# Kernel optimization log

Hardware: AMD Instinct MI355X
Metric: run time of the kernel (lower is better)

## Reference

```python
import jax, jax.numpy as jnp
import numpy as np

NUM_HEADS = 8
N_MOD = 3


def _sinusoidal_pe(seq_len, d_model):
    # standard sinusoidal table [seq_len, d_model]
    pos = np.arange(seq_len, dtype=np.float32)[:, None]
    div = np.exp(np.arange(0, d_model, 2, dtype=np.float32) * (-np.log(10000.0) / d_model))
    pe = np.zeros((seq_len, d_model), dtype=np.float32)
    pe[:, 0::2] = np.sin(pos * div)
    pe[:, 1::2] = np.cos(pos * div)
    return jnp.asarray(pe)


def _attn_mask(dim_x, dim_z, n_mod):
    # additive mask [dim_x, dim_x + n_mod*dim_z]: 0 where allowed, -inf elsewhere
    blocks = [np.eye(dim_x, dtype=np.float32)]
    for _ in range(n_mod):  # all modalities present (mod_list == full_mod)
        p2 = np.zeros((dim_x, dim_z), dtype=np.float32)
        p2[dim_x - dim_z:, :] = np.eye(dim_z, dtype=np.float32)
        blocks.append(p2)
    m = np.concatenate(blocks, axis=1)
    return jnp.asarray(np.where(m < 1, -np.inf, 0.0).astype(np.float32))


def setup_inputs() -> dict:
    key = jax.random.key(0)
    ks = jax.random.split(key, 8)
    bs, en, dx, dz = 32, 256, 512, 256
    state = jax.random.normal(ks[0], (bs, en, dx), jnp.float32)
    obs0 = jax.random.normal(ks[1], (bs, en, dz), jnp.float32)
    obs1 = jax.random.normal(ks[2], (bs, en, dz), jnp.float32)
    obs2 = jax.random.normal(ks[3], (bs, en, dz), jnp.float32)
    Q = jax.random.uniform(ks[4], (dx, en), jnp.float32)  # torch.rand init
    Wq = jax.random.normal(ks[5], (en, en), jnp.float32) / np.sqrt(en)
    Wk = jax.random.normal(ks[6], (en, en), jnp.float32) / np.sqrt(en)
    bq = jnp.zeros((en,), jnp.float32)
    bk = jnp.zeros((en,), jnp.float32)
    return {"state": state, "obs0": obs0, "obs1": obs1, "obs2": obs2,
            "Q": Q, "Wq": Wq, "bq": bq, "Wk": Wk, "bk": bk}


def reference(state, obs0, obs1, obs2, Q, Wq, bq, Wk, bk):
    bs, en, dx = state.shape
    dz = obs0.shape[2]
    obs_list = (obs0, obs1, obs2)
    mask = _attn_mask(dx, dz, N_MOD)            # [dx, L]
    pe = _sinusoidal_pe(bs, en)                 # positions run over batch axis (faithful quirk)

    # mean-center over the ensemble axis
    A = state - jnp.mean(state, axis=1, keepdims=True)          # [bs, en, dx]
    Ys = [o - jnp.mean(o, axis=1, keepdims=True) for o in obs_list]

    # build query / key-value sequences in [tokens, bs, en] layout, add PE, then batch-major
    q = Q[:, None, :] + pe[None, :, :]                          # [dx, bs, en]
    xy = jnp.concatenate([jnp.transpose(A, (2, 0, 1))]
                         + [jnp.transpose(Y, (2, 0, 1)) for Y in Ys], axis=0)
    xy = xy + pe[None, :, :]                                    # [L, bs, en]
    qb = jnp.transpose(q, (1, 0, 2))                            # [bs, dx, en]
    kb = jnp.transpose(xy, (1, 0, 2))                           # [bs, L, en]

    # multi-head masked attention (output path is discarded by the original module,
    # only the attention map is used, so no V/O projection is needed)
    dh = en // NUM_HEADS
    qh = (qb @ Wq + bq).reshape(bs, dx, NUM_HEADS, dh).transpose(0, 2, 1, 3)   # [bs,h,dx,dh]
    kh = (kb @ Wk + bk).reshape(bs, -1, NUM_HEADS, dh).transpose(0, 2, 1, 3)   # [bs,h,L,dh]
    scores = jnp.einsum('bhqd,bhkd->bhqk', qh, kh) / np.sqrt(dh).astype(np.float32)
    scores = scores + mask[None, None, :, :]
    atten = jnp.mean(jax.nn.softmax(scores, axis=-1), axis=1)   # [bs, dx, L]

    # attn-weighted matmul over concatenated raw state+obs
    merge = jnp.concatenate([state, obs0, obs1, obs2], axis=2)  # [bs, en, L]
    new_state = jnp.einsum('bql,bel->beq', atten, merge)        # [bs, en, dx]
    return new_state, atten
```

## Files before the change

kernel.cpp:

```cpp
#include <hip/hip_runtime.h>
#include <math.h>


__global__ __launch_bounds__(256)
void k_uv_copy(const float* __restrict__ Q, const float* __restrict__ Wq,
               const float* __restrict__ bq, const float* __restrict__ state,
               float* __restrict__ uT, float* __restrict__ vT,
               float* __restrict__ out0) {
  const int blk = blockIdx.x;
  const int t = threadIdx.x;
  if (blk < 288) {
    __shared__ float row[256];
    float rv;
    if (blk < 256) {
      rv = Q[(256 + blk) * 256 + t];
    } else {
      const int b = blk - 256;
      const float dv = expf(-9.210340371976184f * (float)((t >> 1) << 1) * (1.0f / 256.0f));
      const float ang = (float)b * dv;
      rv = (t & 1) ? cosf(ang) : sinf(ang);
    }
    row[t] = rv;
    __syncthreads();
    float acc = (blk < 256) ? 0.0f : bq[t];
    for (int e = 0; e < 256; ++e) acc += row[e] * Wq[e * 256 + t];
    if (blk < 256) uT[t * 256 + blk] = acc;
    else           vT[t * 32 + (blk - 256)] = acc;
  } else {
    const int id = blk - 288;
    const int b = id >> 5, eg = id & 31;
    const int r = t >> 5;
    const int c = t & 31;
    const int e = eg * 8 + r;
    const size_t base = ((size_t)(b * 256 + e)) * 512;
    *(float4*)(out0 + base + c * 4)        = *(const float4*)(state + base + c * 4);
    *(float4*)(out0 + base + (c + 32) * 4) = *(const float4*)(state + base + (c + 32) * 4);
  }
}

__global__ __launch_bounds__(256)
void k_w(const float* __restrict__ Wk, const float* __restrict__ uT,
         const float* __restrict__ vT, float* __restrict__ wu2,
         float* __restrict__ wv) {
  const int blk = blockIdx.x;
  const int t = threadIdx.x;
  const int e = blk & 255;
  const int part = blk >> 8;
  __shared__ float wrow[256];
  wrow[t] = Wk[e * 256 + t];
  __syncthreads();
  if (part == 0) {
#pragma unroll
    for (int h = 0; h < 8; ++h) {
      float acc = 0.0f;
#pragma unroll
      for (int d = 0; d < 32; ++d)
        acc += uT[(h * 32 + d) * 256 + t] * wrow[h * 32 + d];
      wu2[(size_t)(h * 256 + e) * 272 + t] = acc;
    }
  } else if (t < 32) {
#pragma unroll
    for (int h = 0; h < 8; ++h) {
      float acc = 0.0f;
#pragma unroll
      for (int d = 0; d < 32; ++d)
        acc += vT[(h * 32 + d) * 32 + t] * wrow[h * 32 + d];
      wv[(t * 8 + h) * 256 + e] = acc;
    }
  }
}

__global__ __launch_bounds__(512)
void k_all(const float* __restrict__ state, const float* __restrict__ o0,
           const float* __restrict__ o1, const float* __restrict__ o2,
           const float* __restrict__ wu2, const float* __restrict__ wv,
           float* __restrict__ out0, float* __restrict__ out1) {
  const int t = threadIdx.x;
  const int jt = blockIdx.x;
  const int b  = blockIdx.y;

  __shared__ float s_data[4][128][17];
  __shared__ float s_wvb[2048];
  __shared__ float s_part[8][16][25];
  __shared__ float s_tot[44][16];
  __shared__ float s_a[16][4];

  for (int i = t; i < 2048; i += 512) s_wvb[i] = wv[b * 2048 + i];

  const int jl = t & 15;
  const int es = (t >> 4) & 15;
  const int hp = t >> 8;
  const int j = jt * 16 + jl;

  float acc[24];
#pragma unroll
  for (int k = 0; k < 24; ++k) acc[k] = 0.f;

  const float* pwu = wu2 + (size_t)hp * 4 * 256 * 272 + j;
  const float* pwvb = s_wvb + hp * 4 * 256;

#pragma unroll
  for (int chunk = 0; chunk < 2; ++chunk) {
    __syncthreads();
#pragma unroll
    for (int rep = 0; rep < 4; ++rep) {
      const int c = t + rep * 512;
      const int m = c >> 9;
      const int r = c & 511;
      const int e = r >> 2;
      const int jq = r & 3;
      const int ge = chunk * 128 + e;
      const int j0 = jt * 16 + jq * 4;
      const float* src;
      if (m == 0)      src = state + ((size_t)(b * 256 + ge)) * 512 + 256 + j0;
      else if (m == 1) src = o0 + ((size_t)(b * 256 + ge)) * 256 + j0;
      else if (m == 2) src = o1 + ((size_t)(b * 256 + ge)) * 256 + j0;
      else             src = o2 + ((size_t)(b * 256 + ge)) * 256 + j0;
      const float4 v4 = *(const float4*)src;
      const int jb = jq * 4;
      s_data[m][e][jb]   = v4.x; s_data[m][e][jb+1] = v4.y;
      s_data[m][e][jb+2] = v4.z; s_data[m][e][jb+3] = v4.w;
    }
    __syncthreads();

#pragma unroll
    for (int it = 0; it < 8; ++it) {
      const int el = it * 16 + es;
      const int e = chunk * 128 + el;
      const float s  = s_data[0][el][jl];
      const float x0 = s_data[1][el][jl];
      const float x1 = s_data[2][el][jl];
      const float x2 = s_data[3][el][jl];
      acc[20] += s; acc[21] += x0; acc[22] += x1; acc[23] += x2;
#pragma unroll
      for (int hh = 0; hh < 4; ++hh) {
        const float w = pwu[(size_t)(hh * 256 + e) * 272] + pwvb[hh * 256 + e];
        acc[hh * 5 + 0] += s * w;  acc[hh * 5 + 1] += x0 * w;
        acc[hh * 5 + 2] += x1 * w; acc[hh * 5 + 3] += x2 * w;
        acc[hh * 5 + 4] += w;
      }
    }
  }

#pragma unroll
  for (int k = 0; k < 24; ++k) {
    acc[k] += __shfl_xor(acc[k], 16);
    acc[k] += __shfl_xor(acc[k], 32);
  }
  if ((t & 48) == 0) {
    const int w = t >> 6;
    float* p = &s_part[w][jl][0];
#pragma unroll
    for (int k = 0; k < 24; ++k) p[k] = acc[k];
  }
  __syncthreads();

  if (t < 16) {
#pragma unroll
    for (int k = 0; k < 20; ++k)
      s_tot[k][t] = s_part[0][t][k] + s_part[1][t][k] + s_part[2][t][k] + s_part[3][t][k];
#pragma unroll
    for (int c = 0; c < 4; ++c)
      s_tot[40 + c][t] = s_part[0][t][20 + c] + s_part[1][t][20 + c] +
                         s_part[2][t][20 + c] + s_part[3][t][20 + c];
  } else if (t >= 256 && t < 272) {
    const int l = t & 15;
#pragma unroll
    for (int k = 0; k < 20; ++k)
      s_tot[20 + k][l] = s_part[4][l][k] + s_part[5][l][k] + s_part[6][l][k] + s_part[7][l][k];
  }
  __syncthreads();

  if (t < 16) {
    float tot[44];
#pragma unroll
    for (int k = 0; k < 44; ++k) tot[k] = s_tot[k][t];
    const float m0 = tot[40] * (1.f / 256.f), m1 = tot[41] * (1.f / 256.f);
    const float m2 = tot[42] * (1.f / 256.f), m3 = tot[43] * (1.f / 256.f);
    const float inv = 0.17677669529663687f;
    float am0 = 0.f, am1 = 0.f, am2 = 0.f, am3 = 0.f;
#pragma unroll
    for (int h = 0; h < 8; ++h) {
      const float dO = tot[h * 5 + 4];
      const float s0 = (tot[h * 5 + 0] - m0 * dO) * inv;
      const float s1 = (tot[h * 5 + 1] - m1 * dO) * inv;
      const float s2 = (tot[h * 5 + 2] - m2 * dO) * inv;
      const float s3 = (tot[h * 5 + 3] - m3 * dO) * inv;
      const float mx = fmaxf(fmaxf(s0, s1), fmaxf(s2, s3));
      const float e0 = expf(s0 - mx), e1 = expf(s1 - mx);
      const float e2 = expf(s2 - mx), e3 = expf(s3 - mx);
      const float r = 1.f / (e0 + e1 + e2 + e3);
      am0 += e0 * r; am1 += e1 * r; am2 += e2 * r; am3 += e3 * r;
    }
    s_a[t][0] = am0 * 0.125f; s_a[t][1] = am1 * 0.125f;
    s_a[t][2] = am2 * 0.125f; s_a[t][3] = am3 * 0.125f;
  }
  __syncthreads();

  {
    const int jl2 = t & 15;
    const int er = t >> 4;
    const float a0 = s_a[jl2][0], a1 = s_a[jl2][1];
    const float a2 = s_a[jl2][2], a3 = s_a[jl2][3];
    const int jj = jt * 16 + jl2;
#pragma unroll
    for (int k = 0; k < 4; ++k) {
      const int e = er + 32 * k;
      const size_t idxS = ((size_t)(b * 256 + e)) * 512 + 256 + jj;
      const size_t idxO = ((size_t)(b * 256 + e)) * 256 + jj;
      out0[idxS] = a0 * state[idxS] + a1 * o0[idxO] + a2 * o1[idxO] + a3 * o2[idxO];
    }
#pragma unroll
    for (int k = 4; k < 8; ++k) {
      const int e = er + 32 * k;
      const int el = e - 128;
      const size_t idxS = ((size_t)(b * 256 + e)) * 512 + 256 + jj;
      out0[idxS] = a0 * s_data[0][el][jl2] + a1 * s_data[1][el][jl2] +
                   a2 * s_data[2][el][jl2] + a3 * s_data[3][el][jl2];
    }
  }

  {
    const int r = t >> 5;
    const int c = t & 31;
    const int j3 = jt * 16 + r;
    const int q = 256 + j3;
    const int comp = j3 & 3;
    const int tc0 = (256 + j3) >> 2, tc1 = (512 + j3) >> 2;
    const int tc2 = (768 + j3) >> 2, tc3 = (1024 + j3) >> 2;
    const float av0 = s_a[r][0], av1 = s_a[r][1];
    const float av2 = s_a[r][2], av3 = s_a[r][3];
    float4* orow = (float4*)(out1 + ((size_t)(b * 512 + q)) * 1280);
#pragma unroll
    for (int k = 0; k < 10; ++k) {
      const int c4 = c + 32 * k;
      float4 o = make_float4(0.f, 0.f, 0.f, 0.f);
      float val = 0.f; bool hit = false;
      if (c4 == tc0)      { val = av0; hit = true; }
      else if (c4 == tc1) { val = av1; hit = true; }
      else if (c4 == tc2) { val = av2; hit = true; }
      else if (c4 == tc3) { val = av3; hit = true; }
      if (hit) {
        if (comp == 0) o.x = val; else if (comp == 1) o.y = val;
        else if (comp == 2) o.z = val; else o.w = val;
      }
      orow[c4] = o;
    }
  }

  {
    const int r = t >> 5;
    const int c = t & 31;
    const int q = jt * 16 + r;
    const int tq = q >> 2;
    const int comp = q & 3;
    float4* orow = (float4*)(out1 + ((size_t)(b * 512 + q)) * 1280);
#pragma unroll
    for (int k = 0; k < 10; ++k) {
      const int c4 = c + 32 * k;
      float4 o = make_float4(0.f, 0.f, 0.f, 0.f);
      if (c4 == tq) {
        if (comp == 0) o.x = 1.f; else if (comp == 1) o.y = 1.f;
        else if (comp == 2) o.z = 1.f; else o.w = 1.f;
      }
      orow[c4] = o;
    }
  }
}

extern "C" void kernel_launch(void* const* d_in, const int* in_sizes, int n_in,
                              void* d_out, int out_size, void* d_ws, size_t ws_size,
                              hipStream_t stream) {
  const float* state = (const float*)d_in[0];
  const float* obs0  = (const float*)d_in[1];
  const float* obs1  = (const float*)d_in[2];
  const float* obs2  = (const float*)d_in[3];
  const float* Q     = (const float*)d_in[4];
  const float* Wq    = (const float*)d_in[5];
  const float* bq    = (const float*)d_in[6];
  const float* Wk    = (const float*)d_in[7];

  float* out0 = (float*)d_out;
  float* out1 = out0 + (size_t)32 * 256 * 512;

  float* ws  = (float*)d_ws;
  float* uT  = ws;
  float* vT  = uT + 65536;
  float* wu2 = vT + 8192;
  float* wv  = wu2 + 557056;

  k_uv_copy<<<1312, 256, 0, stream>>>(Q, Wq, bq, state, uT, vT, out0);
  k_w<<<512, 256, 0, stream>>>(Wk, uT, vT, wu2, wv);
  k_all<<<dim3(16, 32), 512, 0, stream>>>(state, obs0, obs1, obs2, wu2, wv, out0, out1);
}
```

Baseline: 60.66 us.

## Pre-transpose state/obs data to bf16 so the main kernel loads a compact layout

Adds a preprocessing stage in the first kernel that converts the state tail and the three observation tensors to bf16 and transposes them so the ensemble axis is contiguous. The main kernel then loads all 256 ensemble rows for its tile in one pass from this compact buffer, drops the two-chunk reload loop, and computes the weighted output from bf16 values held in shared memory. The intent is to halve the bytes the main kernel reads and to make those loads coalesced. In exchange the first kernel does an extra full read and write pass, and both the scores and the final new_state output are computed from bf16-rounded inputs, which loses precision.

New measurement: 56.70 us. 6.5% less time.

```diff
diff --git a/kernel.cpp b/kernel.cpp
--- a/kernel.cpp
+++ b/kernel.cpp
@@ -1,12 +1,23 @@
 #include <hip/hip_runtime.h>
 #include <math.h>
 
+
+__device__ inline unsigned short f2bf(float f) {
+  unsigned int x = __float_as_uint(f);
+  x += 0x7fffu + ((x >> 16) & 1u);
+  return (unsigned short)(x >> 16);
+}
+__device__ inline float bf2f(unsigned short s) {
+  return __uint_as_float(((unsigned int)s) << 16);
+}
 
 __global__ __launch_bounds__(256)
 void k_uv_copy(const float* __restrict__ Q, const float* __restrict__ Wq,
                const float* __restrict__ bq, const float* __restrict__ state,
+               const float* __restrict__ o0, const float* __restrict__ o1,
+               const float* __restrict__ o2,
                float* __restrict__ uT, float* __restrict__ vT,
-               float* __restrict__ out0) {
+               unsigned short* __restrict__ dT, float* __restrict__ out0) {
   const int blk = blockIdx.x;
   const int t = threadIdx.x;
   if (blk < 288) {
@@ -26,7 +37,7 @@
     for (int e = 0; e < 256; ++e) acc += row[e] * Wq[e * 256 + t];
     if (blk < 256) uT[t * 256 + blk] = acc;
     else           vT[t * 32 + (blk - 256)] = acc;
-  } else {
+  } else if (blk < 1312) {
     const int id = blk - 288;
     const int b = id >> 5, eg = id & 31;
     const int r = t >> 5;
@@ -35,6 +46,41 @@
     const size_t base = ((size_t)(b * 256 + e)) * 512;
     *(float4*)(out0 + base + c * 4)        = *(const float4*)(state + base + c * 4);
     *(float4*)(out0 + base + (c + 32) * 4) = *(const float4*)(state + base + (c + 32) * 4);
+  } else {
+    const int id = blk - 1312;
+    const int b   = id >> 6;
+    const int m   = (id >> 4) & 3;
+    const int jt4 = (id >> 2) & 3;
+    const int et4 = id & 3;
+    __shared__ unsigned short tile[64][72];
+    const float* srcb;
+    int stride, colbase;
+    if (m == 0)      { srcb = state + ((size_t)b * 256) * 512; stride = 512; colbase = 256 + jt4 * 64; }
+    else if (m == 1) { srcb = o0 + ((size_t)b * 256) * 256; stride = 256; colbase = jt4 * 64; }
+    else if (m == 2) { srcb = o1 + ((size_t)b * 256) * 256; stride = 256; colbase = jt4 * 64; }
+    else             { srcb = o2 + ((size_t)b * 256) * 256; stride = 256; colbase = jt4 * 64; }
+#pragma unroll
+    for (int rep = 0; rep < 4; ++rep) {
+      const int c = t + rep * 256;
+      const int f4 = c & 15;
+      const int row = c >> 4;
+      const float4 v = *(const float4*)(srcb + (size_t)(et4 * 64 + row) * stride + colbase + f4 * 4);
+      tile[row][f4 * 4 + 0] = f2bf(v.x); tile[row][f4 * 4 + 1] = f2bf(v.y);
+      tile[row][f4 * 4 + 2] = f2bf(v.z); tile[row][f4 * 4 + 3] = f2bf(v.w);
+    }
+    __syncthreads();
+#pragma unroll
+    for (int rep = 0; rep < 2; ++rep) {
+      const int c = t + rep * 256;
+      const int oct = c & 7;
+      const int jrow = c >> 3;
+      unsigned int p0 = (unsigned int)tile[oct * 8 + 0][jrow] | ((unsigned int)tile[oct * 8 + 1][jrow] << 16);
+      unsigned int p1 = (unsigned int)tile[oct * 8 + 2][jrow] | ((unsigned int)tile[oct * 8 + 3][jrow] << 16);
+      unsigned int p2 = (unsigned int)tile[oct * 8 + 4][jrow] | ((unsigned int)tile[oct * 8 + 5][jrow] << 16);
+      unsigned int p3 = (unsigned int)tile[oct * 8 + 6][jrow] | ((unsigned int)tile[oct * 8 + 7][jrow] << 16);
+      uint4 o = make_uint4(p0, p1, p2, p3);
+      *(uint4*)(dT + ((size_t)((b * 4 + m) * 256 + jt4 * 64 + jrow)) * 256 + et4 * 64 + oct * 8) = o;
+    }
   }
 }
 
@@ -71,15 +117,14 @@
 }
 
 __global__ __launch_bounds__(512)
-void k_all(const float* __restrict__ state, const float* __restrict__ o0,
-           const float* __restrict__ o1, const float* __restrict__ o2,
+void k_all(const unsigned short* __restrict__ dT,
            const float* __restrict__ wu2, const float* __restrict__ wv,
            float* __restrict__ out0, float* __restrict__ out1) {
   const int t = threadIdx.x;
   const int jt = blockIdx.x;
   const int b  = blockIdx.y;
 
-  __shared__ float s_data[4][128][17];
+  __shared__ unsigned short s_data[4][256][17];
   __shared__ float s_wvb[2048];
   __shared__ float s_part[8][16][25];
   __shared__ float s_tot[44][16];
@@ -87,6 +132,26 @@
 
   for (int i = t; i < 2048; i += 512) s_wvb[i] = wv[b * 2048 + i];
 
+#pragma unroll
+  for (int rep = 0; rep < 4; ++rep) {
+    const int c = t + rep * 512;
+    const int m = c >> 9;
+    const int jr = (c >> 5) & 15;
+    const int oct = c & 31;
+    const uint4 v = *(const uint4*)(dT +
+        ((size_t)((b * 4 + m) * 256 + jt * 16 + jr)) * 256 + oct * 8);
+    const int e0 = oct * 8;
+    s_data[m][e0 + 0][jr] = (unsigned short)(v.x & 0xffff);
+    s_data[m][e0 + 1][jr] = (unsigned short)(v.x >> 16);
+    s_data[m][e0 + 2][jr] = (unsigned short)(v.y & 0xffff);
+    s_data[m][e0 + 3][jr] = (unsigned short)(v.y >> 16);
+    s_data[m][e0 + 4][jr] = (unsigned short)(v.z & 0xffff);
+    s_data[m][e0 + 5][jr] = (unsigned short)(v.z >> 16);
+    s_data[m][e0 + 6][jr] = (unsigned short)(v.w & 0xffff);
+    s_data[m][e0 + 7][jr] = (unsigned short)(v.w >> 16);
+  }
+  __syncthreads();
+
   const int jl = t & 15;
   const int es = (t >> 4) & 15;
   const int hp = t >> 8;
@@ -100,45 +165,19 @@
   const float* pwvb = s_wvb + hp * 4 * 256;
 
 #pragma unroll
-  for (int chunk = 0; chunk < 2; ++chunk) {
-    __syncthreads();
-#pragma unroll
-    for (int rep = 0; rep < 4; ++rep) {
-      const int c = t + rep * 512;
-      const int m = c >> 9;
-      const int r = c & 511;
-      const int e = r >> 2;
-      const int jq = r & 3;
-      const int ge = chunk * 128 + e;
-      const int j0 = jt * 16 + jq * 4;
-      const float* src;
-      if (m == 0)      src = state + ((size_t)(b * 256 + ge)) * 512 + 256 + j0;
-      else if (m == 1) src = o0 + ((size_t)(b * 256 + ge)) * 256 + j0;
-      else if (m == 2) src = o1 + ((size_t)(b * 256 + ge)) * 256 + j0;
-      else             src = o2 + ((size_t)(b * 256 + ge)) * 256 + j0;
-      const float4 v4 = *(const float4*)src;
-      const int jb = jq * 4;
-      s_data[m][e][jb]   = v4.x; s_data[m][e][jb+1] = v4.y;
-      s_data[m][e][jb+2] = v4.z; s_data[m][e][jb+3] = v4.w;
-    }
-    __syncthreads();
-
-#pragma unroll
-    for (int it = 0; it < 8; ++it) {
-      const int el = it * 16 + es;
-      const int e = chunk * 128 + el;
-      const float s  = s_data[0][el][jl];
-      const float x0 = s_data[1][el][jl];
-      const float x1 = s_data[2][el][jl];
-      const float x2 = s_data[3][el][jl];
-      acc[20] += s; acc[21] += x0; acc[22] += x1; acc[23] += x2;
-#pragma unroll
-      for (int hh = 0; hh < 4; ++hh) {
-        const float w = pwu[(size_t)(hh * 256 + e) * 272] + pwvb[hh * 256 + e];
-        acc[hh * 5 + 0] += s * w;  acc[hh * 5 + 1] += x0 * w;
-        acc[hh * 5 + 2] += x1 * w; acc[hh * 5 + 3] += x2 * w;
-        acc[hh * 5 + 4] += w;
-      }
+  for (int it = 0; it < 16; ++it) {
+    const int e = it * 16 + es;
+    const float s  = bf2f(s_data[0][e][jl]);
+    const float x0 = bf2f(s_data[1][e][jl]);
+    const float x1 = bf2f(s_data[2][e][jl]);
+    const float x2 = bf2f(s_data[3][e][jl]);
+    acc[20] += s; acc[21] += x0; acc[22] += x1; acc[23] += x2;
+#pragma unroll
+    for (int hh = 0; hh < 4; ++hh) {
+      const float w = pwu[(size_t)(hh * 256 + e) * 272] + pwvb[hh * 256 + e];
+      acc[hh * 5 + 0] += s * w;  acc[hh * 5 + 1] += x0 * w;
+      acc[hh * 5 + 2] += x1 * w; acc[hh * 5 + 3] += x2 * w;
+      acc[hh * 5 + 4] += w;
     }
   }
 
@@ -204,19 +243,11 @@
     const float a2 = s_a[jl2][2], a3 = s_a[jl2][3];
     const int jj = jt * 16 + jl2;
 #pragma unroll
-    for (int k = 0; k < 4; ++k) {
+    for (int k = 0; k < 8; ++k) {
       const int e = er + 32 * k;
       const size_t idxS = ((size_t)(b * 256 + e)) * 512 + 256 + jj;
-      const size_t idxO = ((size_t)(b * 256 + e)) * 256 + jj;
-      out0[idxS] = a0 * state[idxS] + a1 * o0[idxO] + a2 * o1[idxO] + a3 * o2[idxO];
-    }
-#pragma unroll
-    for (int k = 4; k < 8; ++k) {
-      const int e = er + 32 * k;
-      const int el = e - 128;
-      const size_t idxS = ((size_t)(b * 256 + e)) * 512 + 256 + jj;
-      out0[idxS] = a0 * s_data[0][el][jl2] + a1 * s_data[1][el][jl2] +
-                   a2 * s_data[2][el][jl2] + a3 * s_data[3][el][jl2];
+      out0[idxS] = a0 * bf2f(s_data[0][e][jl2]) + a1 * bf2f(s_data[1][e][jl2]) +
+                   a2 * bf2f(s_data[2][e][jl2]) + a3 * bf2f(s_data[3][e][jl2]);
     }
   }
 
@@ -288,8 +319,10 @@
   float* vT  = uT + 65536;
   float* wu2 = vT + 8192;
   float* wv  = wu2 + 557056;
-
-  k_uv_copy<<<1312, 256, 0, stream>>>(Q, Wq, bq, state, uT, vT, out0);
+  unsigned short* dT = (unsigned short*)(wv + 65536);
+
+  k_uv_copy<<<3360, 256, 0, stream>>>(Q, Wq, bq, state, obs0, obs1, obs2,
+                                      uT, vT, dT, out0);
   k_w<<<512, 256, 0, stream>>>(Wk, uT, vT, wu2, wv);
-  k_all<<<dim3(16, 32), 512, 0, stream>>>(state, obs0, obs1, obs2, wu2, wv, out0, out1);
-}
+  k_all<<<dim3(16, 32), 512, 0, stream>>>(dT, wu2, wv, out0, out1);
+}
```
